# Kernel optimization log

Hardware: AMD Instinct MI355X
Metric: run time of the kernel (lower is better)

## Reference

```python
import jax, jax.numpy as jnp
import numpy as np

B, T, D = 4096, 8, 2048
EPS = 1e-5


def setup_inputs() -> dict:
    key = jax.random.key(0)
    ks = jax.random.split(key, 7)
    s = 1.0 / np.sqrt(D)  # xavier-ish scale
    return {
        "H": jax.random.normal(ks[0], (B, T, D), jnp.float32),
        "Wq": jax.random.normal(ks[1], (T, D, D), jnp.float32) * s,
        "Wk": jax.random.normal(ks[2], (D, D), jnp.float32) * s,
        "Wv": jax.random.normal(ks[3], (D, D), jnp.float32) * s,
        "Wg": jax.random.normal(ks[4], (T, D, D), jnp.float32) * s,
        "bg": jnp.zeros((T, D), jnp.float32),
        "gamma": jnp.ones((T, D), jnp.float32),
        "beta": jnp.zeros((T, D), jnp.float32),
    }


def reference(H, Wq, Wk, Wv, Wg, bg, gamma, beta):
    # H: (B, T, D) = stacked task_reprs. Linear uses y = x @ W.T.
    scale = jnp.sqrt(jnp.asarray(D, H.dtype))
    K = jnp.einsum('bsd,ed->bse', H, Wk)          # (B, T, D) shared keys
    V = jnp.einsum('bsd,ed->bse', H, Wv)          # (B, T, D) shared values
    Q = jnp.einsum('btd,ted->bte', H, Wq)         # per-task query projection
    scores = jnp.einsum('bte,bse->bts', Q, K) / scale  # (B, T, T)
    attn = jax.nn.softmax(scores, axis=-1)
    ctx = jnp.einsum('bts,bse->bte', attn, V)     # (B, T, D)
    # dropout is identity at eval time
    g = jax.nn.sigmoid(jnp.einsum('btd,ted->bte', H, Wg) + bg)  # per-task gate
    x = H + g * ctx                               # gated residual
    mu = jnp.mean(x, axis=-1, keepdims=True)
    var = jnp.var(x, axis=-1, keepdims=True)
    out = (x - mu) / jnp.sqrt(var + EPS) * gamma + beta  # per-task LayerNorm
    return out
```

## Files before the change

### kernel.cpp

```cpp
#include <hip/hip_runtime.h>
#include <cstdint>

typedef unsigned short u16;
typedef uint32_t u32;
typedef float f32x4 __attribute__((ext_vector_type(4)));
typedef __bf16 bf16x8 __attribute__((ext_vector_type(8)));

#define GLDS16(gp, lp)                                                                   \
  __builtin_amdgcn_global_load_lds((const __attribute__((address_space(1))) void*)(gp),  \
                                   (__attribute__((address_space(3))) void*)(lp), 16, 0, 0)

__device__ __forceinline__ float blo(u32 u) { return __uint_as_float(u << 16); }
__device__ __forceinline__ float bhi(u32 u) { return __uint_as_float(u & 0xFFFF0000u); }
__device__ __forceinline__ u16 f2b(float f) {
  u32 u = __float_as_uint(f);
  u32 r = u + 0x7FFFu + ((u >> 16) & 1u);
  return (u16)(r >> 16);
}

__global__ __launch_bounds__(256) void ctil_cvt_f2b(
    const float* __restrict__ in, u16* __restrict__ out, long n)
{
  long i = ((long)blockIdx.x * blockDim.x + threadIdx.x) * 8;
  const long stride = (long)gridDim.x * blockDim.x * 8;
  for (; i < n; i += stride) {
    float4 a = *reinterpret_cast<const float4*>(in + i);
    float4 b = *reinterpret_cast<const float4*>(in + i + 4);
    uint4 o;
    o.x = (u32)f2b(a.x) | ((u32)f2b(a.y) << 16);
    o.y = (u32)f2b(a.z) | ((u32)f2b(a.w) << 16);
    o.z = (u32)f2b(b.x) | ((u32)f2b(b.y) << 16);
    o.w = (u32)f2b(b.z) | ((u32)f2b(b.w) << 16);
    *reinterpret_cast<uint4*>(out + i) = o;
  }
}

__global__ __launch_bounds__(512, 2) void ctil_gemm256(
    const u16* __restrict__ Hb, const u16* __restrict__ Wqb,
    const u16* __restrict__ Wkb, const u16* __restrict__ Wvb,
    const u16* __restrict__ Wgb,
    u16* __restrict__ Kb, u16* __restrict__ Vb,
    u16* __restrict__ Qb, u16* __restrict__ Gb,
    int zbase)
{
  const int z = blockIdx.z + zbase;
  const u16* A;
  const u16* W;
  u16* C;
  int lda, ldc;
  if (z < 2) {
    A = Hb; lda = 2048; ldc = 2048;
    W = (z == 0) ? Wkb : Wvb;
    C = (z == 0) ? Kb : Vb;
  } else {
    const int t = (z - 2) & 7;
    A = Hb + t * 2048; lda = 16384; ldc = 16384;
    W = ((z < 10) ? Wqb : Wgb) + (size_t)t * (size_t)(2048 * 2048);
    C = ((z < 10) ? Qb : Gb) + t * 2048;
  }
  const int bm = blockIdx.x, bn = blockIdx.y;
  const int tid = (int)threadIdx.x;
  const int lane = tid & 63, wid = tid >> 6;
  const int wm = wid >> 2, wn = wid & 3;

  __shared__ __align__(16) u16 As[2][16384];
  __shared__ __align__(16) u16 Bs[2][16384];

  const int srl = lane >> 3;
  const int sq  = (lane & 7) ^ srl;
  const u16* Ag = A + (size_t)(bm * 256 + wid * 8 + srl) * lda + sq * 8;
  const u16* Bg = W + (size_t)(bn * 256 + wid * 8 + srl) * 2048 + sq * 8;

#define STAGE(buf, kt, h)                                                     \
  do {                                                                        \
    GLDS16(Ag + (size_t)((h) * 64) * lda + (kt) * 64,                         \
           &As[buf][((h) * 64 + wid * 8) * 64]);                              \
    GLDS16(Bg + (size_t)((h) * 64) * 2048 + (kt) * 64,                        \
           &Bs[buf][((h) * 64 + wid * 8) * 64]);                              \
  } while (0)

  const int la = lane & 15, g = lane >> 4, x = lane & 7;
  const int arow = wm * 128 + la;
  const int brow = wn * 64 + la;
  const int sl0 = (g ^ x) << 3;
  const int sl1 = ((4 | g) ^ x) << 3;

  bf16x8 aR[4][2];
  bf16x8 bR[2][2][2];
  f32x4 acc[8][4] = {};

#define DSA(buf, mh)                                                          \
  do {                                                                        \
    _Pragma("unroll") for (int j = 0; j < 4; ++j) {                           \
      const int r_ = (arow + (mh) * 64 + j * 16) * 64;                        \
      aR[j][0] = *reinterpret_cast<const bf16x8*>(&As[buf][r_ + sl0]);        \
      aR[j][1] = *reinterpret_cast<const bf16x8*>(&As[buf][r_ + sl1]);        \
    }                                                                         \
  } while (0)

#define DSB(buf, nh)                                                          \
  do {                                                                        \
    _Pragma("unroll") for (int j = 0; j < 2; ++j) {                           \
      const int r_ = (brow + (nh) * 32 + j * 16) * 64;                        \
      bR[nh][j][0] = *reinterpret_cast<const bf16x8*>(&Bs[buf][r_ + sl0]);    \
      bR[nh][j][1] = *reinterpret_cast<const bf16x8*>(&Bs[buf][r_ + sl1]);    \
    }                                                                         \
  } while (0)

#define MFMA16(mh, nh)                                                        \
  do {                                                                        \
    _Pragma("unroll") for (int j = 0; j < 4; ++j)                             \
    _Pragma("unroll") for (int jj = 0; jj < 2; ++jj)                          \
    _Pragma("unroll") for (int ks = 0; ks < 2; ++ks)                          \
      acc[(mh) * 4 + j][(nh) * 2 + jj] =                                      \
          __builtin_amdgcn_mfma_f32_16x16x32_bf16(                            \
              aR[j][ks], bR[nh][jj][ks], acc[(mh) * 4 + j][(nh) * 2 + jj],    \
              0, 0, 0);                                                       \
  } while (0)

#define BAR()                                                                 \
  do {                                                                        \
    __builtin_amdgcn_s_barrier();                                             \
    asm volatile("" ::: "memory");                                            \
  } while (0)
#define LGKM0()                                                               \
  do {                                                                        \
    asm volatile("s_waitcnt lgkmcnt(0)" ::: "memory");                        \
    __builtin_amdgcn_sched_barrier(0);                                        \
  } while (0)

#pragma unroll
  for (int h = 0; h < 4; ++h) STAGE(0, 0, h);

#pragma unroll 1
  for (int it = 0; it < 16; ++it) {
    const int k1 = 2 * it + 1, k2 = 2 * it + 2;
    const bool nl = (it < 15);
    STAGE(1, k1, 0);
    asm volatile("s_waitcnt vmcnt(2)" ::: "memory");
    BAR();
    DSA(0, 0); DSB(0, 0);
    LGKM0();
    __builtin_amdgcn_s_setprio(1); MFMA16(0, 0); __builtin_amdgcn_s_setprio(0);
    BAR();
    DSB(0, 1);
    STAGE(1, k1, 1);
    BAR(); LGKM0();
    __builtin_amdgcn_s_setprio(1); MFMA16(0, 1); __builtin_amdgcn_s_setprio(0);
    BAR();
    DSA(0, 1);
    STAGE(1, k1, 2);
    BAR(); LGKM0();
    __builtin_amdgcn_s_setprio(1); MFMA16(1, 1); __builtin_amdgcn_s_setprio(0);
    BAR();
    STAGE(1, k1, 3);
    BAR(); LGKM0();
    __builtin_amdgcn_s_setprio(1); MFMA16(1, 0); __builtin_amdgcn_s_setprio(0);
    BAR();
    if (nl) {
      STAGE(0, k2, 0);
      asm volatile("s_waitcnt vmcnt(2)" ::: "memory");
    } else {
      asm volatile("s_waitcnt vmcnt(0)" ::: "memory");
    }
    BAR();
    DSA(1, 0); DSB(1, 0);
    LGKM0();
    __builtin_amdgcn_s_setprio(1); MFMA16(0, 0); __builtin_amdgcn_s_setprio(0);
    BAR();
    DSB(1, 1);
    if (nl) STAGE(0, k2, 1);
    BAR(); LGKM0();
    __builtin_amdgcn_s_setprio(1); MFMA16(0, 1); __builtin_amdgcn_s_setprio(0);
    BAR();
    DSA(1, 1);
    if (nl) STAGE(0, k2, 2);
    BAR(); LGKM0();
    __builtin_amdgcn_s_setprio(1); MFMA16(1, 1); __builtin_amdgcn_s_setprio(0);
    BAR();
    if (nl) STAGE(0, k2, 3);
    BAR(); LGKM0();
    __builtin_amdgcn_s_setprio(1); MFMA16(1, 0); __builtin_amdgcn_s_setprio(0);
    BAR();
  }

  const int cl = lane & 15, cq = lane >> 4;
#pragma unroll
  for (int mf = 0; mf < 8; ++mf) {
#pragma unroll
    for (int r = 0; r < 4; ++r) {
      const int row = bm * 256 + wm * 128 + mf * 16 + cq * 4 + r;
      u16* Cr = C + (size_t)row * ldc + bn * 256 + wn * 64 + cl;
#pragma unroll
      for (int nf = 0; nf < 4; ++nf)
        Cr[nf * 16] = f2b(acc[mf][nf][r]);
    }
  }
#undef STAGE
#undef DSA
#undef DSB
#undef MFMA16
#undef BAR
#undef LGKM0
}

__global__ __launch_bounds__(256) void ctil_epilogue(
    const u16* __restrict__ Hb, const u16* __restrict__ Kb,
    const u16* __restrict__ Vb, const u16* __restrict__ Qb,
    const u16* __restrict__ Gb, const float* __restrict__ bgp,
    const float* __restrict__ gap, const float* __restrict__ bep,
    float* __restrict__ Out)
{
  const int b = blockIdx.x;
  const int tid = (int)threadIdx.x;
  const int lane = tid & 63, wid = tid >> 6;
  const size_t rbase = (size_t)b * 16384;
  const int e0 = tid * 8;

  __shared__ float red[256];
  __shared__ float r1s[4], r2s[4];

  u32 qw[8][4], kw[8][4];
#pragma unroll
  for (int t = 0; t < 8; ++t) {
    uint4 v = *reinterpret_cast<const uint4*>(Qb + rbase + t * 2048 + e0);
    qw[t][0] = v.x; qw[t][1] = v.y; qw[t][2] = v.z; qw[t][3] = v.w;
    uint4 w = *reinterpret_cast<const uint4*>(Kb + rbase + t * 2048 + e0);
    kw[t][0] = w.x; kw[t][1] = w.y; kw[t][2] = w.z; kw[t][3] = w.w;
  }

  float sc[64];
#pragma unroll
  for (int p = 0; p < 64; ++p) sc[p] = 0.f;

#pragma unroll
  for (int c = 0; c < 4; ++c) {
    float ql[8], qh[8], kl[8], kh[8];
#pragma unroll
    for (int t = 0; t < 8; ++t) {
      ql[t] = blo(qw[t][c]); qh[t] = bhi(qw[t][c]);
      kl[t] = blo(kw[t][c]); kh[t] = bhi(kw[t][c]);
    }
#pragma unroll
    for (int t = 0; t < 8; ++t)
#pragma unroll
      for (int s = 0; s < 8; ++s)
        sc[t * 8 + s] += ql[t] * kl[s] + qh[t] * kh[s];
  }

#pragma unroll
  for (int p = 0; p < 64; ++p) {
    float v = sc[p];
#pragma unroll
    for (int m = 1; m < 64; m <<= 1) v += __shfl_xor(v, m, 64);
    sc[p] = v;
  }
  if (lane == 0) {
#pragma unroll
    for (int p = 0; p < 64; ++p) red[wid * 64 + p] = sc[p];
  }
  __syncthreads();

  const float INVS = 0.022097086912079608f;
#pragma unroll
  for (int p = 0; p < 64; ++p)
    sc[p] = (red[p] + red[64 + p] + red[128 + p] + red[192 + p]) * INVS;

#pragma unroll
  for (int t = 0; t < 8; ++t) {
    float m = sc[t * 8];
#pragma unroll
    for (int s = 1; s < 8; ++s) m = fmaxf(m, sc[t * 8 + s]);
    float l = 0.f;
#pragma unroll
    for (int s = 0; s < 8; ++s) {
      float e = __expf(sc[t * 8 + s] - m);
      sc[t * 8 + s] = e;
      l += e;
    }
    float inv = 1.f / l;
#pragma unroll
    for (int s = 0; s < 8; ++s) sc[t * 8 + s] *= inv;
  }

  u32 vw[8][4];
#pragma unroll
  for (int s = 0; s < 8; ++s) {
    uint4 v = *reinterpret_cast<const uint4*>(Vb + rbase + s * 2048 + e0);
    vw[s][0] = v.x; vw[s][1] = v.y; vw[s][2] = v.z; vw[s][3] = v.w;
  }

  for (int t = 0; t < 8; ++t) {
    float cx[8];
#pragma unroll
    for (int j = 0; j < 8; ++j) cx[j] = 0.f;
#pragma unroll
    for (int s = 0; s < 8; ++s) {
      float a = sc[t * 8 + s];
#pragma unroll
      for (int c = 0; c < 4; ++c) {
        cx[2 * c]     += a * blo(vw[s][c]);
        cx[2 * c + 1] += a * bhi(vw[s][c]);
      }
    }
    uint4 gu = *reinterpret_cast<const uint4*>(Gb + rbase + t * 2048 + e0);
    uint4 hu = *reinterpret_cast<const uint4*>(Hb + rbase + t * 2048 + e0);
    u32 ga[4] = {gu.x, gu.y, gu.z, gu.w};
    u32 ha[4] = {hu.x, hu.y, hu.z, hu.w};
    float bgv[8];
    *reinterpret_cast<float4*>(&bgv[0]) = *reinterpret_cast<const float4*>(bgp + t * 2048 + e0);
    *reinterpret_cast<float4*>(&bgv[4]) = *reinterpret_cast<const float4*>(bgp + t * 2048 + e0 + 4);
    float x[8];
    float s1 = 0.f, s2 = 0.f;
#pragma unroll
    for (int c = 0; c < 4; ++c) {
      float gl = blo(ga[c]) + bgv[2 * c];
      float gh = bhi(ga[c]) + bgv[2 * c + 1];
      float sgl = 1.f / (1.f + __expf(-gl));
      float sgh = 1.f / (1.f + __expf(-gh));
      float xl = blo(ha[c]) + sgl * cx[2 * c];
      float xh = bhi(ha[c]) + sgh * cx[2 * c + 1];
      x[2 * c] = xl; x[2 * c + 1] = xh;
      s1 += xl + xh;
      s2 += xl * xl + xh * xh;
    }
#pragma unroll
    for (int m = 1; m < 64; m <<= 1) {
      s1 += __shfl_xor(s1, m, 64);
      s2 += __shfl_xor(s2, m, 64);
    }
    if (lane == 0) { r1s[wid] = s1; r2s[wid] = s2; }
    __syncthreads();
    const float invD = 1.f / 2048.f;
    float S1 = r1s[0] + r1s[1] + r1s[2] + r1s[3];
    float S2 = r2s[0] + r2s[1] + r2s[2] + r2s[3];
    float mu = S1 * invD;
    float var = S2 * invD - mu * mu;
    float rstd = rsqrtf(var + 1e-5f);
    float gmv[8], btv[8];
    *reinterpret_cast<float4*>(&gmv[0]) = *reinterpret_cast<const float4*>(gap + t * 2048 + e0);
    *reinterpret_cast<float4*>(&gmv[4]) = *reinterpret_cast<const float4*>(gap + t * 2048 + e0 + 4);
    *reinterpret_cast<float4*>(&btv[0]) = *reinterpret_cast<const float4*>(bep + t * 2048 + e0);
    *reinterpret_cast<float4*>(&btv[4]) = *reinterpret_cast<const float4*>(bep + t * 2048 + e0 + 4);
    float4 o1, o2;
    o1.x = (x[0] - mu) * rstd * gmv[0] + btv[0];
    o1.y = (x[1] - mu) * rstd * gmv[1] + btv[1];
    o1.z = (x[2] - mu) * rstd * gmv[2] + btv[2];
    o1.w = (x[3] - mu) * rstd * gmv[3] + btv[3];
    o2.x = (x[4] - mu) * rstd * gmv[4] + btv[4];
    o2.y = (x[5] - mu) * rstd * gmv[5] + btv[5];
    o2.z = (x[6] - mu) * rstd * gmv[6] + btv[6];
    o2.w = (x[7] - mu) * rstd * gmv[7] + btv[7];
    *reinterpret_cast<float4*>(Out + rbase + t * 2048 + e0) = o1;
    *reinterpret_cast<float4*>(Out + rbase + t * 2048 + e0 + 4) = o2;
    __syncthreads();
  }
}

extern "C" void kernel_launch(void* const* d_in, const int* in_sizes, int n_in,
                              void* d_out, int out_size, void* d_ws, size_t ws_size,
                              hipStream_t stream)
{
  const float* H  = (const float*)d_in[0];
  const float* Wq = (const float*)d_in[1];
  const float* Wk = (const float*)d_in[2];
  const float* Wv = (const float*)d_in[3];
  const float* Wg = (const float*)d_in[4];
  const float* bg = (const float*)d_in[5];
  const float* ga = (const float*)d_in[6];
  const float* be = (const float*)d_in[7];
  float* Out = (float*)d_out;

  const size_t NWQ = 33554432, NWK = 4194304;
  u16* Wqb = (u16*)d_ws;
  u16* Wgb = Wqb + NWQ;
  u16* Wkb = Wgb + NWQ;
  u16* Wvb = Wkb + NWK;
  u16* chunkbase = Wvb + NWK;

  const size_t fixed = 150994944ull;
  int nch = 1;
  while (nch < 16 && fixed + (size_t)(4096 / nch) * 163840ull > ws_size) nch <<= 1;
  const int CB = 4096 / nch;

  u16* Hb = chunkbase;
  u16* Kw = Hb + (size_t)CB * 16384;
  u16* Vw = Kw + (size_t)CB * 16384;
  u16* Gw = Vw + (size_t)CB * 16384;
  u16* Qw = Gw + (size_t)CB * 16384;

  ctil_cvt_f2b<<<2048, 256, 0, stream>>>(Wq, Wqb, (long)NWQ);
  ctil_cvt_f2b<<<2048, 256, 0, stream>>>(Wg, Wgb, (long)NWQ);
  ctil_cvt_f2b<<<512, 256, 0, stream>>>(Wk, Wkb, (long)NWK);
  ctil_cvt_f2b<<<512, 256, 0, stream>>>(Wv, Wvb, (long)NWK);

  for (int c = 0; c < nch; ++c) {
    const size_t off = (size_t)c * (size_t)CB * 16384;
    ctil_cvt_f2b<<<2048, 256, 0, stream>>>(H + off, Hb, (long)CB * 16384);
    ctil_gemm256<<<dim3(CB / 32, 8, 2), 512, 0, stream>>>(
        Hb, Wqb, Wkb, Wvb, Wgb, Kw, Vw, Qw, Gw, 0);
    ctil_gemm256<<<dim3(CB / 256, 8, 16), 512, 0, stream>>>(
        Hb, Wqb, Wkb, Wvb, Wgb, Kw, Vw, Qw, Gw, 2);
    ctil_epilogue<<<dim3(CB), 256, 0, stream>>>(
        Hb, Kw, Vw, Qw, Gw, bg, ga, be, Out + off);
  }
}
```

Before: 1.717 ms.

## Deepen GEMM global-to-LDS prefetch and drop redundant barriers in main loop

Reschedules the double-buffered bf16 GEMM main loop so that half of the next buffer's tiles are issued before the loop, and the rest are issued earlier within each half-iteration, in pairs. The wait thresholds are relaxed from vmcnt(2) to vmcnt(8), which keeps more global-to-LDS loads in flight. One barrier plus LDS wait per half-iteration is removed by placing the stage issue directly before the final MFMA block. The goal is to hide more memory latency behind MFMA work and cut synchronization overhead. The cost is more outstanding loads and a more delicate LDS overwrite ordering that depends on register-resident fragments.

```diff
diff --git a/kernel.cpp b/kernel.cpp
--- a/kernel.cpp
+++ b/kernel.cpp
@@ -128,59 +128,59 @@
     asm volatile("s_waitcnt lgkmcnt(0)" ::: "memory");                        \
     __builtin_amdgcn_sched_barrier(0);                                        \
   } while (0)
+#define PRIO_ON()  __builtin_amdgcn_s_setprio(1)
+#define PRIO_OFF() __builtin_amdgcn_s_setprio(0)
 
 #pragma unroll
   for (int h = 0; h < 4; ++h) STAGE(0, 0, h);
+  STAGE(1, 1, 0);
+  STAGE(1, 1, 1);
 
 #pragma unroll 1
   for (int it = 0; it < 16; ++it) {
-    const int k1 = 2 * it + 1, k2 = 2 * it + 2;
+    const int k1 = 2 * it + 1, k2 = 2 * it + 2, k3 = 2 * it + 3;
     const bool nl = (it < 15);
-    STAGE(1, k1, 0);
-    asm volatile("s_waitcnt vmcnt(2)" ::: "memory");
+    STAGE(1, k1, 2);
+    STAGE(1, k1, 3);
+    asm volatile("s_waitcnt vmcnt(8)" ::: "memory");
     BAR();
     DSA(0, 0); DSB(0, 0);
     LGKM0();
-    __builtin_amdgcn_s_setprio(1); MFMA16(0, 0); __builtin_amdgcn_s_setprio(0);
+    PRIO_ON(); MFMA16(0, 0); PRIO_OFF();
     BAR();
     DSB(0, 1);
-    STAGE(1, k1, 1);
     BAR(); LGKM0();
-    __builtin_amdgcn_s_setprio(1); MFMA16(0, 1); __builtin_amdgcn_s_setprio(0);
+    PRIO_ON(); MFMA16(0, 1); PRIO_OFF();
     BAR();
     DSA(0, 1);
-    STAGE(1, k1, 2);
     BAR(); LGKM0();
-    __builtin_amdgcn_s_setprio(1); MFMA16(1, 1); __builtin_amdgcn_s_setprio(0);
-    BAR();
-    STAGE(1, k1, 3);
-    BAR(); LGKM0();
-    __builtin_amdgcn_s_setprio(1); MFMA16(1, 0); __builtin_amdgcn_s_setprio(0);
+    PRIO_ON(); MFMA16(1, 1); PRIO_OFF();
+    BAR();
+    if (nl) { STAGE(0, k2, 0); STAGE(0, k2, 1); }
+    PRIO_ON(); MFMA16(1, 0); PRIO_OFF();
     BAR();
     if (nl) {
-      STAGE(0, k2, 0);
-      asm volatile("s_waitcnt vmcnt(2)" ::: "memory");
+      STAGE(0, k2, 2);
+      STAGE(0, k2, 3);
+      asm volatile("s_waitcnt vmcnt(8)" ::: "memory");
     } else {
       asm volatile("s_waitcnt vmcnt(0)" ::: "memory");
     }
     BAR();
     DSA(1, 0); DSB(1, 0);
     LGKM0();
-    __builtin_amdgcn_s_setprio(1); MFMA16(0, 0); __builtin_amdgcn_s_setprio(0);
+    PRIO_ON(); MFMA16(0, 0); PRIO_OFF();
     BAR();
     DSB(1, 1);
-    if (nl) STAGE(0, k2, 1);
     BAR(); LGKM0();
-    __builtin_amdgcn_s_setprio(1); MFMA16(0, 1); __builtin_amdgcn_s_setprio(0);
+    PRIO_ON(); MFMA16(0, 1); PRIO_OFF();
     BAR();
     DSA(1, 1);
-    if (nl) STAGE(0, k2, 2);
     BAR(); LGKM0();
-    __builtin_amdgcn_s_setprio(1); MFMA16(1, 1); __builtin_amdgcn_s_setprio(0);
-    BAR();
-    if (nl) STAGE(0, k2, 3);
-    BAR(); LGKM0();
-    __builtin_amdgcn_s_setprio(1); MFMA16(1, 0); __builtin_amdgcn_s_setprio(0);
+    PRIO_ON(); MFMA16(1, 1); PRIO_OFF();
+    BAR();
+    if (nl) { STAGE(1, k3, 0); STAGE(1, k3, 1); }
+    PRIO_ON(); MFMA16(1, 0); PRIO_OFF();
     BAR();
   }
 
```

Result: faster. 1.637 ms (-4.7%).
